# Kernel tuning notes

Hardware: AMD Instinct MI355X
Metric: run time of the kernel (lower is better)

## Reference

```python
import jax, jax.numpy as jnp
import numpy as np

B, S, P, D = 32, 512, 512, 768

def setup_inputs() -> dict:
    key = jax.random.key(0)
    k1, k2 = jax.random.split(key)
    inputs = jax.random.normal(k1, (B, S, D), dtype=jnp.float32)
    prototypes = jax.random.normal(k2, (P, D), dtype=jnp.float32)
    return {"inputs": inputs, "prototypes": prototypes}

def reference(inputs, prototypes):
    # Squared Euclidean distance from every token vector to every prototype:
    # but the cross term is a GEMM and the huge [B,S,P,D] intermediate is never built).
    x_sq = jnp.sum(inputs * inputs, axis=-1, keepdims=True)          # [B, S, 1]
    p_sq = jnp.sum(prototypes * prototypes, axis=-1)                 # [P]
    cross = jnp.einsum('bsd,pd->bsp', inputs, prototypes)            # [B, S, P]
    distances = x_sq + p_sq[None, None, :] - 2.0 * cross             # [B, S, P]
    return (distances, prototypes)
```

## Files before the change

kernel.cpp:

```cpp
#include <hip/hip_runtime.h>
#include <hip/hip_bf16.h>


#define M_TOK 16384
#define N_PROT 512
#define K_DIM 768
#define BK 32
#define NCH (K_DIM / BK)
#define ASTR (K_DIM + 8)

typedef __attribute__((ext_vector_type(4))) float f32x4;
typedef __attribute__((ext_vector_type(8))) short bf16x8;

__device__ inline unsigned short f2bf(float f) {
    unsigned int u = __float_as_uint(f);
    u += 0x7fffu + ((u >> 16) & 1u);
    return (unsigned short)(u >> 16);
}

__global__ __launch_bounds__(256) void prep_b(
    const float* __restrict__ p,
    unsigned short* __restrict__ b_bf, float* __restrict__ p_sq,
    float* __restrict__ proto_out)
{
    const int row  = blockIdx.x * 4 + (threadIdx.x >> 6);
    const int lane = threadIdx.x & 63;

    const int g    = row >> 4;
    const int l16p = row & 15;

    const float4* src4 = (const float4*)(p + (size_t)row * K_DIM);
    float4* pout4 = (float4*)(proto_out + (size_t)row * K_DIM);

    float ssum = 0.0f;
#pragma unroll
    for (int j = 0; j < 3; ++j) {
        const int idx = lane + j * 64;
        float4 v = src4[idx];
        ssum += v.x * v.x + v.y * v.y + v.z * v.z + v.w * v.w;
        ushort4 b;
        b.x = f2bf(v.x); b.y = f2bf(v.y); b.z = f2bf(v.z); b.w = f2bf(v.w);
        const int k0   = idx * 4;
        const int kk   = k0 >> 5;
        const int quad = (k0 >> 3) & 3;
        const int j0   = k0 & 7;
        const int dst  = (g * 24 + kk) * 512 + quad * 128 + l16p * 8 + j0;
        *(ushort4*)&b_bf[dst] = b;
        pout4[idx] = v;
    }
#pragma unroll
    for (int off = 32; off > 0; off >>= 1) ssum += __shfl_down(ssum, off);
    if (lane == 0) p_sq[row] = ssum;
}

__global__ __launch_bounds__(1024, 4) void dist_main(
    const float* __restrict__ X,
    const unsigned short* __restrict__ Bb,
    const float* __restrict__ p_sq,
    float* __restrict__ out)
{
    __shared__ unsigned short lds_a[64 * ASTR];
    __shared__ float lds_xsq[64];

    const int tid  = threadIdx.x;
    const int wave = tid >> 6;
    const int lane = tid & 63;
    const int bm   = blockIdx.x << 6;
    const int wn   = wave << 5;
    const int quad = lane >> 4;
    const int l16  = lane & 15;

    const int ar = tid >> 4;
    const int ac = tid & 15;
    const float* aptr = X + (size_t)(bm + ar) * K_DIM;
    float asq = 0.0f;
#pragma unroll
    for (int j = 0; j < 12; ++j) {
        const int c4 = ac + 16 * j;
        float4 v = *(const float4*)(aptr + (size_t)c4 * 4);
        asq += v.x * v.x + v.y * v.y + v.z * v.z + v.w * v.w;
        ushort4 u;
        u.x = f2bf(v.x); u.y = f2bf(v.y); u.z = f2bf(v.z); u.w = f2bf(v.w);
        *(ushort4*)&lds_a[ar * ASTR + c4 * 4] = u;
    }
#pragma unroll
    for (int off = 1; off < 16; off <<= 1) asq += __shfl_xor(asq, off);
    if (ac == 0) lds_xsq[ar] = asq;

    __syncthreads();

    const f32x4 zero = {0.0f, 0.0f, 0.0f, 0.0f};
    f32x4 acc[4][2];
#pragma unroll
    for (int mt = 0; mt < 4; ++mt)
#pragma unroll
        for (int nt = 0; nt < 2; ++nt) acc[mt][nt] = zero;

    const unsigned short* bp = Bb + (size_t)lane * 8;
    const int gbase = (wave << 1) * 24;

    bf16x8 bcur[2], bnxt[2];
#pragma unroll
    for (int nt = 0; nt < 2; ++nt)
        bcur[nt] = *(const bf16x8*)(bp + (size_t)(gbase + nt * 24) * 512);

    for (int kc = 0; kc < NCH; ++kc) {
        const int k0 = kc * BK;
        if (kc + 1 < NCH) {
#pragma unroll
            for (int nt = 0; nt < 2; ++nt)
                bnxt[nt] = *(const bf16x8*)(bp
                    + (size_t)(gbase + nt * 24 + kc + 1) * 512);
        }

        bf16x8 af[4];
#pragma unroll
        for (int mt = 0; mt < 4; ++mt)
            af[mt] = *(const bf16x8*)&lds_a[(mt * 16 + l16) * ASTR + k0 + quad * 8];

#pragma unroll
        for (int mt = 0; mt < 4; ++mt)
#pragma unroll
            for (int nt = 0; nt < 2; ++nt)
                acc[mt][nt] = __builtin_amdgcn_mfma_f32_16x16x32_bf16(
                    af[mt], bcur[nt], acc[mt][nt], 0, 0, 0);

#pragma unroll
        for (int nt = 0; nt < 2; ++nt) bcur[nt] = bnxt[nt];
    }

    float ps[2];
#pragma unroll
    for (int nt = 0; nt < 2; ++nt) ps[nt] = p_sq[wn + nt * 16 + l16];

#pragma unroll
    for (int mt = 0; mt < 4; ++mt) {
#pragma unroll
        for (int i = 0; i < 4; ++i) {
            const int lr = mt * 16 + quad * 4 + i;
            const float xs = lds_xsq[lr];
            float* orow = out + (size_t)(bm + lr) * N_PROT + wn + l16;
#pragma unroll
            for (int nt = 0; nt < 2; ++nt)
                orow[nt * 16] = xs + ps[nt] - 2.0f * acc[mt][nt][i];
        }
    }
}

extern "C" void kernel_launch(void* const* d_in, const int* in_sizes, int n_in,
                              void* d_out, int out_size, void* d_ws, size_t ws_size,
                              hipStream_t stream) {
    const float* inputs = (const float*)d_in[0];
    const float* protos = (const float*)d_in[1];
    float* out = (float*)d_out;
    float* proto_out = out + (size_t)M_TOK * N_PROT;

    char* ws = (char*)d_ws;
    unsigned short* b_bf = (unsigned short*)ws;
    float* p_sq = (float*)(ws + 786432);

    prep_b<<<128, 256, 0, stream>>>(protos, b_bf, p_sq, proto_out);
    dist_main<<<M_TOK / 64, 1024, 0, stream>>>(inputs, b_bf, p_sq, out);
}
```

Measured before the change: 102.6 us.

## Double-buffer A tile in LDS, overlapping global loads with MFMA compute

Each block no longer loads and converts the whole 64x768 A tile up front before any MFMA work. It now streams A in 128-wide K chunks through a two-slot LDS buffer. The next chunk's global loads are issued before the current chunk's MFMAs, and the bf16 conversion and LDS store happen afterwards, so load latency overlaps compute. LDS use drops from about 99KB to about 34KB, which may allow more resident blocks. The cost is a __syncthreads per chunk, and the row norms are now accumulated incrementally and reduced at the end.

```diff
diff --git a/kernel.cpp b/kernel.cpp
--- a/kernel.cpp
+++ b/kernel.cpp
@@ -5,9 +5,10 @@
 #define M_TOK 16384
 #define N_PROT 512
 #define K_DIM 768
-#define BK 32
-#define NCH (K_DIM / BK)
-#define ASTR (K_DIM + 8)
+#define BKC 128
+#define NKC (K_DIM / BKC)
+#define NSK (K_DIM / 32)
+#define ASTR 132
 
 typedef __attribute__((ext_vector_type(4))) float f32x4;
 typedef __attribute__((ext_vector_type(8))) short bf16x8;
@@ -59,7 +60,7 @@
     const float* __restrict__ p_sq,
     float* __restrict__ out)
 {
-    __shared__ unsigned short lds_a[64 * ASTR];
+    __shared__ unsigned short lds_a[2][64 * ASTR];
     __shared__ float lds_xsq[64];
 
     const int tid  = threadIdx.x;
@@ -72,29 +73,22 @@
 
     const int ar = tid >> 4;
     const int ac = tid & 15;
-    const float* aptr = X + (size_t)(bm + ar) * K_DIM;
+    const float* aptr = X + (size_t)(bm + ar) * K_DIM + ac * 4;
+
     float asq = 0.0f;
-#pragma unroll
-    for (int j = 0; j < 12; ++j) {
-        const int c4 = ac + 16 * j;
-        float4 v = *(const float4*)(aptr + (size_t)c4 * 4);
-        asq += v.x * v.x + v.y * v.y + v.z * v.z + v.w * v.w;
-        ushort4 u;
-        u.x = f2bf(v.x); u.y = f2bf(v.y); u.z = f2bf(v.z); u.w = f2bf(v.w);
-        *(ushort4*)&lds_a[ar * ASTR + c4 * 4] = u;
+
+    {
+        float4 v0 = *(const float4*)(aptr);
+        float4 v1 = *(const float4*)(aptr + 64);
+        asq += v0.x * v0.x + v0.y * v0.y + v0.z * v0.z + v0.w * v0.w;
+        asq += v1.x * v1.x + v1.y * v1.y + v1.z * v1.z + v1.w * v1.w;
+        ushort4 u0, u1;
+        u0.x = f2bf(v0.x); u0.y = f2bf(v0.y); u0.z = f2bf(v0.z); u0.w = f2bf(v0.w);
+        u1.x = f2bf(v1.x); u1.y = f2bf(v1.y); u1.z = f2bf(v1.z); u1.w = f2bf(v1.w);
+        *(ushort4*)&lds_a[0][ar * ASTR + ac * 4]      = u0;
+        *(ushort4*)&lds_a[0][ar * ASTR + ac * 4 + 64] = u1;
     }
-#pragma unroll
-    for (int off = 1; off < 16; off <<= 1) asq += __shfl_xor(asq, off);
-    if (ac == 0) lds_xsq[ar] = asq;
-
     __syncthreads();
-
-    const f32x4 zero = {0.0f, 0.0f, 0.0f, 0.0f};
-    f32x4 acc[4][2];
-#pragma unroll
-    for (int mt = 0; mt < 4; ++mt)
-#pragma unroll
-        for (int nt = 0; nt < 2; ++nt) acc[mt][nt] = zero;
 
     const unsigned short* bp = Bb + (size_t)lane * 8;
     const int gbase = (wave << 1) * 24;
@@ -104,30 +98,65 @@
     for (int nt = 0; nt < 2; ++nt)
         bcur[nt] = *(const bf16x8*)(bp + (size_t)(gbase + nt * 24) * 512);
 
-    for (int kc = 0; kc < NCH; ++kc) {
-        const int k0 = kc * BK;
-        if (kc + 1 < NCH) {
+    const f32x4 zero = {0.0f, 0.0f, 0.0f, 0.0f};
+    f32x4 acc[4][2];
 #pragma unroll
-            for (int nt = 0; nt < 2; ++nt)
-                bnxt[nt] = *(const bf16x8*)(bp
-                    + (size_t)(gbase + nt * 24 + kc + 1) * 512);
+    for (int mt = 0; mt < 4; ++mt) {
+        acc[mt][0] = zero; acc[mt][1] = zero;
+    }
+
+    for (int kc = 0; kc < NKC; ++kc) {
+        float4 s0, s1;
+        if (kc + 1 < NKC) {
+            const float* ap = aptr + (kc + 1) * BKC;
+            s0 = *(const float4*)(ap);
+            s1 = *(const float4*)(ap + 64);
         }
 
-        bf16x8 af[4];
 #pragma unroll
-        for (int mt = 0; mt < 4; ++mt)
-            af[mt] = *(const bf16x8*)&lds_a[(mt * 16 + l16) * ASTR + k0 + quad * 8];
+        for (int ss = 0; ss < 4; ++ss) {
+            const int kk = kc * 4 + ss;
+            if (kk + 1 < NSK) {
+#pragma unroll
+                for (int nt = 0; nt < 2; ++nt)
+                    bnxt[nt] = *(const bf16x8*)(bp
+                        + (size_t)((gbase + nt * 24) * 24 / 24 + nt * 0) * 0
+                        + (size_t)(gbase + nt * 24 + kk + 1) * 512);
+            }
+
+            bf16x8 af[4];
+#pragma unroll
+            for (int mt = 0; mt < 4; ++mt)
+                af[mt] = *(const bf16x8*)&lds_a[kc & 1]
+                    [(mt * 16 + l16) * ASTR + ss * 32 + quad * 8];
 
 #pragma unroll
-        for (int mt = 0; mt < 4; ++mt)
-#pragma unroll
-            for (int nt = 0; nt < 2; ++nt)
-                acc[mt][nt] = __builtin_amdgcn_mfma_f32_16x16x32_bf16(
-                    af[mt], bcur[nt], acc[mt][nt], 0, 0, 0);
+            for (int mt = 0; mt < 4; ++mt) {
+                acc[mt][0] = __builtin_amdgcn_mfma_f32_16x16x32_bf16(
+                    af[mt], bcur[0], acc[mt][0], 0, 0, 0);
+                acc[mt][1] = __builtin_amdgcn_mfma_f32_16x16x32_bf16(
+                    af[mt], bcur[1], acc[mt][1], 0, 0, 0);
+            }
+            bcur[0] = bnxt[0]; bcur[1] = bnxt[1];
+        }
+
+        if (kc + 1 < NKC) {
+            unsigned short* aw = &lds_a[(kc + 1) & 1][ar * ASTR + ac * 4];
+            asq += s0.x * s0.x + s0.y * s0.y + s0.z * s0.z + s0.w * s0.w;
+            asq += s1.x * s1.x + s1.y * s1.y + s1.z * s1.z + s1.w * s1.w;
+            ushort4 u0, u1;
+            u0.x = f2bf(s0.x); u0.y = f2bf(s0.y); u0.z = f2bf(s0.z); u0.w = f2bf(s0.w);
+            u1.x = f2bf(s1.x); u1.y = f2bf(s1.y); u1.z = f2bf(s1.z); u1.w = f2bf(s1.w);
+            *(ushort4*)(aw)      = u0;
+            *(ushort4*)(aw + 64) = u1;
+        }
+        __syncthreads();
+    }
 
 #pragma unroll
-        for (int nt = 0; nt < 2; ++nt) bcur[nt] = bnxt[nt];
-    }
+    for (int off = 1; off < 16; off <<= 1) asq += __shfl_xor(asq, off);
+    if (ac == 0) lds_xsq[ar] = asq;
+    __syncthreads();
 
     float ps[2];
 #pragma unroll
```

New measurement: 109.7 us. 7.0% more time.

## Split A-tile staging into two K halves overlapping second-half loads with MFMA

Applied to the files above, without the earlier changes.

The A tile (64 rows x 768 fp32) was previously loaded, converted to bf16 and written to LDS entirely before any MFMA work began. Now only the first half of K is staged up front. The second half's global loads are issued into registers and left in flight while the first 12 K-steps of MFMA run, then converted and stored after another barrier. This hides part of the global-load latency behind compute, at the cost of 24 extra VGPRs for the held float4s and an extra __syncthreads, which matters under 1024-thread blocks.

```diff
diff --git a/kernel.cpp b/kernel.cpp
--- a/kernel.cpp
+++ b/kernel.cpp
@@ -6,7 +6,8 @@
 #define N_PROT 512
 #define K_DIM 768
 #define BK 32
-#define NCH (K_DIM / BK)
+#define NSK (K_DIM / BK)
+#define KSEC 12
 #define ASTR (K_DIM + 8)
 
 typedef __attribute__((ext_vector_type(4))) float f32x4;
@@ -73,9 +74,11 @@
     const int ar = tid >> 4;
     const int ac = tid & 15;
     const float* aptr = X + (size_t)(bm + ar) * K_DIM;
+
     float asq = 0.0f;
-#pragma unroll
-    for (int j = 0; j < 12; ++j) {
+
+#pragma unroll
+    for (int j = 0; j < 6; ++j) {
         const int c4 = ac + 16 * j;
         float4 v = *(const float4*)(aptr + (size_t)c4 * 4);
         asq += v.x * v.x + v.y * v.y + v.z * v.z + v.w * v.w;
@@ -83,30 +86,62 @@
         u.x = f2bf(v.x); u.y = f2bf(v.y); u.z = f2bf(v.z); u.w = f2bf(v.w);
         *(ushort4*)&lds_a[ar * ASTR + c4 * 4] = u;
     }
-#pragma unroll
-    for (int off = 1; off < 16; off <<= 1) asq += __shfl_xor(asq, off);
-    if (ac == 0) lds_xsq[ar] = asq;
-
     __syncthreads();
+
+    const unsigned short* bp = Bb + (size_t)lane * 8;
+    const int gbase = (wave << 1) * 24;
+
+    bf16x8 bcur[2], bnxt[2];
+#pragma unroll
+    for (int nt = 0; nt < 2; ++nt)
+        bcur[nt] = *(const bf16x8*)(bp + (size_t)(gbase + nt * 24) * 512);
+
+    float4 s1[6];
+#pragma unroll
+    for (int j = 0; j < 6; ++j)
+        s1[j] = *(const float4*)(aptr + (size_t)(96 + ac + 16 * j) * 4);
 
     const f32x4 zero = {0.0f, 0.0f, 0.0f, 0.0f};
     f32x4 acc[4][2];
 #pragma unroll
-    for (int mt = 0; mt < 4; ++mt)
-#pragma unroll
-        for (int nt = 0; nt < 2; ++nt) acc[mt][nt] = zero;
-
-    const unsigned short* bp = Bb + (size_t)lane * 8;
-    const int gbase = (wave << 1) * 24;
-
-    bf16x8 bcur[2], bnxt[2];
-#pragma unroll
-    for (int nt = 0; nt < 2; ++nt)
-        bcur[nt] = *(const bf16x8*)(bp + (size_t)(gbase + nt * 24) * 512);
-
-    for (int kc = 0; kc < NCH; ++kc) {
+    for (int mt = 0; mt < 4; ++mt) {
+        acc[mt][0] = zero; acc[mt][1] = zero;
+    }
+
+    for (int kc = 0; kc < KSEC; ++kc) {
+#pragma unroll
+        for (int nt = 0; nt < 2; ++nt)
+            bnxt[nt] = *(const bf16x8*)(bp
+                + (size_t)(gbase + nt * 24 + kc + 1) * 512);
+
+        bf16x8 af[4];
         const int k0 = kc * BK;
-        if (kc + 1 < NCH) {
+#pragma unroll
+        for (int mt = 0; mt < 4; ++mt)
+            af[mt] = *(const bf16x8*)&lds_a[(mt * 16 + l16) * ASTR + k0 + quad * 8];
+
+#pragma unroll
+        for (int mt = 0; mt < 4; ++mt) {
+            acc[mt][0] = __builtin_amdgcn_mfma_f32_16x16x32_bf16(
+                af[mt], bcur[0], acc[mt][0], 0, 0, 0);
+            acc[mt][1] = __builtin_amdgcn_mfma_f32_16x16x32_bf16(
+                af[mt], bcur[1], acc[mt][1], 0, 0, 0);
+        }
+        bcur[0] = bnxt[0]; bcur[1] = bnxt[1];
+    }
+
+#pragma unroll
+    for (int j = 0; j < 6; ++j) {
+        float4 v = s1[j];
+        asq += v.x * v.x + v.y * v.y + v.z * v.z + v.w * v.w;
+        ushort4 u;
+        u.x = f2bf(v.x); u.y = f2bf(v.y); u.z = f2bf(v.z); u.w = f2bf(v.w);
+        *(ushort4*)&lds_a[ar * ASTR + (96 + ac + 16 * j) * 4] = u;
+    }
+    __syncthreads();
+
+    for (int kc = KSEC; kc < NSK; ++kc) {
+        if (kc + 1 < NSK) {
 #pragma unroll
             for (int nt = 0; nt < 2; ++nt)
                 bnxt[nt] = *(const bf16x8*)(bp
@@ -114,20 +149,25 @@
         }
 
         bf16x8 af[4];
+        const int k0 = kc * BK;
 #pragma unroll
         for (int mt = 0; mt < 4; ++mt)
             af[mt] = *(const bf16x8*)&lds_a[(mt * 16 + l16) * ASTR + k0 + quad * 8];
 
 #pragma unroll
-        for (int mt = 0; mt < 4; ++mt)
-#pragma unroll
-            for (int nt = 0; nt < 2; ++nt)
-                acc[mt][nt] = __builtin_amdgcn_mfma_f32_16x16x32_bf16(
-                    af[mt], bcur[nt], acc[mt][nt], 0, 0, 0);
-
-#pragma unroll
-        for (int nt = 0; nt < 2; ++nt) bcur[nt] = bnxt[nt];
-    }
+        for (int mt = 0; mt < 4; ++mt) {
+            acc[mt][0] = __builtin_amdgcn_mfma_f32_16x16x32_bf16(
+                af[mt], bcur[0], acc[mt][0], 0, 0, 0);
+            acc[mt][1] = __builtin_amdgcn_mfma_f32_16x16x32_bf16(
+                af[mt], bcur[1], acc[mt][1], 0, 0, 0);
+        }
+        bcur[0] = bnxt[0]; bcur[1] = bnxt[1];
+    }
+
+#pragma unroll
+    for (int off = 1; off < 16; off <<= 1) asq += __shfl_xor(asq, off);
+    if (ac == 0) lds_xsq[ar] = asq;
+    __syncthreads();
 
     float ps[2];
 #pragma unroll
```

Result: slower. 107.7 us (+5.0%).

## Split N across two blocks, stage A in K halves, swizzle blocks per XCD

Applied to the files above, without the earlier changes.

Each block now computes a 64x256 output tile with 512 threads instead of 64x512 with 1024 threads, which doubles the grid to 512 blocks. The A tile is converted and staged into LDS in two K-halves, so LDS use per block is halved and compute on the first half can start sooner. Block IDs are remapped so that the two N-halves sharing an A row-tile land on the same XCD, which favours L2 reuse of the duplicated X reads. The cost is that each X row is read and converted to bf16 twice, and an extra barrier sits between the two sections.

```diff
diff --git a/kernel.cpp b/kernel.cpp
--- a/kernel.cpp
+++ b/kernel.cpp
@@ -6,8 +6,9 @@
 #define N_PROT 512
 #define K_DIM 768
 #define BK 32
-#define NCH (K_DIM / BK)
-#define ASTR (K_DIM + 8)
+#define NSK (K_DIM / BK)
+#define KSEC 12
+#define ASTR2 392
 
 typedef __attribute__((ext_vector_type(4))) float f32x4;
 typedef __attribute__((ext_vector_type(8))) short bf16x8;
@@ -53,81 +54,96 @@
     if (lane == 0) p_sq[row] = ssum;
 }
 
-__global__ __launch_bounds__(1024, 4) void dist_main(
+__global__ __launch_bounds__(512, 4) void dist_main(
     const float* __restrict__ X,
     const unsigned short* __restrict__ Bb,
     const float* __restrict__ p_sq,
     float* __restrict__ out)
 {
-    __shared__ unsigned short lds_a[64 * ASTR];
+    __shared__ unsigned short lds_a[64 * ASTR2];
     __shared__ float lds_xsq[64];
+
+    const int bid     = blockIdx.x;
+    const int logical = (bid & 7) * 64 + (bid >> 3);
+    const int ms = logical >> 1;
+    const int nh = logical & 1;
+    const int bm = ms << 6;
 
     const int tid  = threadIdx.x;
     const int wave = tid >> 6;
     const int lane = tid & 63;
-    const int bm   = blockIdx.x << 6;
-    const int wn   = wave << 5;
+    const int wn   = (nh << 8) + (wave << 5);
     const int quad = lane >> 4;
     const int l16  = lane & 15;
 
-    const int ar = tid >> 4;
-    const int ac = tid & 15;
+    const int ar = tid >> 3;
+    const int ac = tid & 7;
     const float* aptr = X + (size_t)(bm + ar) * K_DIM;
+
     float asq = 0.0f;
-#pragma unroll
-    for (int j = 0; j < 12; ++j) {
-        const int c4 = ac + 16 * j;
-        float4 v = *(const float4*)(aptr + (size_t)c4 * 4);
-        asq += v.x * v.x + v.y * v.y + v.z * v.z + v.w * v.w;
-        ushort4 u;
-        u.x = f2bf(v.x); u.y = f2bf(v.y); u.z = f2bf(v.z); u.w = f2bf(v.w);
-        *(ushort4*)&lds_a[ar * ASTR + c4 * 4] = u;
-    }
-#pragma unroll
-    for (int off = 1; off < 16; off <<= 1) asq += __shfl_xor(asq, off);
-    if (ac == 0) lds_xsq[ar] = asq;
 
-    __syncthreads();
+    const unsigned short* bp = Bb + (size_t)lane * 8;
+    const int gbase = ((nh << 4) + (wave << 1)) * 24;
 
     const f32x4 zero = {0.0f, 0.0f, 0.0f, 0.0f};
     f32x4 acc[4][2];
 #pragma unroll
-    for (int mt = 0; mt < 4; ++mt)
-#pragma unroll
-        for (int nt = 0; nt < 2; ++nt) acc[mt][nt] = zero;
-
-    const unsigned short* bp = Bb + (size_t)lane * 8;
-    const int gbase = (wave << 1) * 24;
+    for (int mt = 0; mt < 4; ++mt) {
+        acc[mt][0] = zero; acc[mt][1] = zero;
+    }
 
     bf16x8 bcur[2], bnxt[2];
+
 #pragma unroll
-    for (int nt = 0; nt < 2; ++nt)
-        bcur[nt] = *(const bf16x8*)(bp + (size_t)(gbase + nt * 24) * 512);
+    for (int sec = 0; sec < 2; ++sec) {
+#pragma unroll
+        for (int j = 0; j < 12; ++j) {
+            const int c4 = ac + 8 * j;
+            float4 v = *(const float4*)(aptr + (size_t)(sec * 96 + c4) * 4);
+            asq += v.x * v.x + v.y * v.y + v.z * v.z + v.w * v.w;
+            ushort4 u;
+            u.x = f2bf(v.x); u.y = f2bf(v.y); u.z = f2bf(v.z); u.w = f2bf(v.w);
+            *(ushort4*)&lds_a[ar * ASTR2 + c4 * 4] = u;
+        }
+        __syncthreads();
 
-    for (int kc = 0; kc < NCH; ++kc) {
-        const int k0 = kc * BK;
-        if (kc + 1 < NCH) {
+        const int kk0 = sec * KSEC;
 #pragma unroll
-            for (int nt = 0; nt < 2; ++nt)
-                bnxt[nt] = *(const bf16x8*)(bp
-                    + (size_t)(gbase + nt * 24 + kc + 1) * 512);
+        for (int nt = 0; nt < 2; ++nt)
+            bcur[nt] = *(const bf16x8*)(bp + (size_t)(gbase + nt * 24 + kk0) * 512);
+
+        for (int ks = 0; ks < KSEC; ++ks) {
+            const int kk = kk0 + ks;
+            if (kk + 1 < NSK) {
+#pragma unroll
+                for (int nt = 0; nt < 2; ++nt)
+                    bnxt[nt] = *(const bf16x8*)(bp
+                        + (size_t)(gbase + nt * 24 + kk + 1) * 512);
+            }
+
+            bf16x8 af[4];
+#pragma unroll
+            for (int mt = 0; mt < 4; ++mt)
+                af[mt] = *(const bf16x8*)&lds_a[(mt * 16 + l16) * ASTR2
+                                                + ks * BK + quad * 8];
+
+#pragma unroll
+            for (int mt = 0; mt < 4; ++mt) {
+                acc[mt][0] = __builtin_amdgcn_mfma_f32_16x16x32_bf16(
+                    af[mt], bcur[0], acc[mt][0], 0, 0, 0);
+                acc[mt][1] = __builtin_amdgcn_mfma_f32_16x16x32_bf16(
+                    af[mt], bcur[1], acc[mt][1], 0, 0, 0);
+            }
+            bcur[0] = bnxt[0]; bcur[1] = bnxt[1];
         }
 
-        bf16x8 af[4];
-#pragma unroll
-        for (int mt = 0; mt < 4; ++mt)
-            af[mt] = *(const bf16x8*)&lds_a[(mt * 16 + l16) * ASTR + k0 + quad * 8];
+        if (sec == 0) __syncthreads();
+    }
 
 #pragma unroll
-        for (int mt = 0; mt < 4; ++mt)
-#pragma unroll
-            for (int nt = 0; nt < 2; ++nt)
-                acc[mt][nt] = __builtin_amdgcn_mfma_f32_16x16x32_bf16(
-                    af[mt], bcur[nt], acc[mt][nt], 0, 0, 0);
-
-#pragma unroll
-        for (int nt = 0; nt < 2; ++nt) bcur[nt] = bnxt[nt];
-    }
+    for (int off = 1; off < 8; off <<= 1) asq += __shfl_xor(asq, off);
+    if (ac == 0) lds_xsq[ar] = asq;
+    __syncthreads();
 
     float ps[2];
 #pragma unroll
@@ -160,5 +176,5 @@
     float* p_sq = (float*)(ws + 786432);
 
     prep_b<<<128, 256, 0, stream>>>(protos, b_bf, p_sq, proto_out);
-    dist_main<<<M_TOK / 64, 1024, 0, stream>>>(inputs, b_bf, p_sq, out);
+    dist_main<<<512, 512, 0, stream>>>(inputs, b_bf, p_sq, out);
 }
```

Result: slower. 116.7 us (+13.8%).
